# Performance work log

Measured on AMD Instinct MI355X. Metric: run time of the kernel, lower is better.

## Reference

```python
import jax, jax.numpy as jnp
import numpy as np

B, N, S = 8, 8192, 128


def setup_inputs() -> dict:
    key = jax.random.key(0)
    k1, k2, k3 = jax.random.split(key, 3)
    densities = jax.random.uniform(k1, (B, N, S, 1), dtype=jnp.float32)
    rgbs = jax.random.uniform(k2, (B, N, S, 3), dtype=jnp.float32)
    # sample distances along each ray must be increasing -> sort along S
    t_vals = jnp.sort(jax.random.uniform(k3, (B, N, S), dtype=jnp.float32) * 6.0, axis=-1)
    return {"densities": densities, "rgbs": rgbs, "t_vals": t_vals}


def reference(densities, rgbs, t_vals):
    INF_DELTA = 1e10
    EPS = 1e-10
    sigma = densities[..., 0]                                   # [B,N,S]
    deltas = t_vals[..., 1:] - t_vals[..., :-1]
    deltas = jnp.concatenate(
        [deltas, jnp.full_like(deltas[..., :1], INF_DELTA)], axis=-1
    )                                                           # [B,N,S]
    alpha = 1.0 - jnp.exp(-sigma * deltas)                      # [B,N,S]
    # exclusive cumprod of (1 - alpha): T_i = prod_{j<i} (1 - alpha_j)
    trans = jnp.cumprod(
        jnp.concatenate([jnp.ones_like(alpha[..., :1]), 1.0 - alpha + EPS], axis=-1),
        axis=-1,
    )[..., :-1]                                                 # [B,N,S]
    weights = trans * alpha                                     # [B,N,S]
    rgb = jnp.einsum("bns,bnsc->bnc", weights, rgbs)            # [B,N,3]
    depth = jnp.sum(weights * t_vals, axis=-1, keepdims=True)   # [B,N,1]
    accumulation = jnp.sum(weights, axis=-1, keepdims=True)     # [B,N,1]
    return rgb, weights, depth, accumulation
```

## Files before the change

kernel.cpp:

```cpp
#include <hip/hip_runtime.h>


namespace {
constexpr int kB = 8;
constexpr int kN = 8192;
constexpr int kS = 128;
constexpr int kRays = kB * kN;
constexpr int kWavesPerBlock = 4;

__global__ __launch_bounds__(256) void volrender_kernel(
    const float* __restrict__ dens,
    const float* __restrict__ rgbs,
    const float* __restrict__ tvals,
    float* __restrict__ out_rgb,
    float* __restrict__ out_w,
    float* __restrict__ out_depth,
    float* __restrict__ out_acc)
{
    const int lane = threadIdx.x & 63;
    const int wave = threadIdx.x >> 6;
    const int ray  = blockIdx.x * kWavesPerBlock + wave;

    const long base = (long)ray * kS;

    const float2 t2 = *(const float2*)(tvals + base + lane * 2);
    const float2 sg = *(const float2*)(dens  + base + lane * 2);
    const float* rp = rgbs + (long)ray * kS * 3 + lane * 6;
    const float2 ra = *(const float2*)(rp + 0);
    const float2 rb = *(const float2*)(rp + 2);
    const float2 rc = *(const float2*)(rp + 4);

    const float t_next = __shfl_down(t2.x, 1);
    const float d0 = t2.y - t2.x;
    const float d1 = (lane == 63) ? 1e10f : (t_next - t2.y);

    const float e0 = expf(-sg.x * d0);
    const float e1 = expf(-sg.y * d1);
    const float a0 = 1.0f - e0;
    const float a1 = 1.0f - e1;
    const float f0 = e0 + 1e-10f;
    const float f1 = e1 + 1e-10f;

    float p = f0 * f1;
    #pragma unroll
    for (int off = 1; off < 64; off <<= 1) {
        const float q = __shfl_up(p, off);
        if (lane >= off) p *= q;
    }
    float excl = __shfl_up(p, 1);
    if (lane == 0) excl = 1.0f;

    const float T0 = excl;
    const float T1 = excl * f0;
    const float w0 = T0 * a0;
    const float w1 = T1 * a1;

    *(float2*)(out_w + base + lane * 2) = make_float2(w0, w1);

    float cr  = w0 * ra.x + w1 * rb.y;
    float cg  = w0 * ra.y + w1 * rc.x;
    float cb  = w0 * rb.x + w1 * rc.y;
    float dep = w0 * t2.x + w1 * t2.y;
    float acc = w0 + w1;

    #pragma unroll
    for (int off = 32; off; off >>= 1) {
        cr  += __shfl_down(cr,  off);
        cg  += __shfl_down(cg,  off);
        cb  += __shfl_down(cb,  off);
        dep += __shfl_down(dep, off);
        acc += __shfl_down(acc, off);
    }

    if (lane == 0) {
        out_rgb[ray * 3 + 0] = cr;
        out_rgb[ray * 3 + 1] = cg;
        out_rgb[ray * 3 + 2] = cb;
        out_depth[ray] = dep;
        out_acc[ray]   = acc;
    }
}
}

extern "C" void kernel_launch(void* const* d_in, const int* in_sizes, int n_in,
                              void* d_out, int out_size, void* d_ws, size_t ws_size,
                              hipStream_t stream) {
    const float* dens  = (const float*)d_in[0];
    const float* rgbs  = (const float*)d_in[1];
    const float* tvals = (const float*)d_in[2];

    float* out       = (float*)d_out;
    float* out_rgb   = out;
    float* out_w     = out_rgb + (long)kRays * 3;
    float* out_depth = out_w + (long)kRays * kS;
    float* out_acc   = out_depth + kRays;

    const dim3 grid(kRays / kWavesPerBlock);
    const dim3 block(kWavesPerBlock * 64);
    hipLaunchKernelGGL(volrender_kernel, grid, block, 0, stream,
                       dens, rgbs, tvals, out_rgb, out_w, out_depth, out_acc);
}
```

Before: 34.84 us.

## Process two rays per wave with four samples per lane using float4 loads

Each 64-lane wave now handles two rays: 32 lanes per ray, 4 samples per lane. Loads and the weights store widen to float4, and the prefix-product scan and reductions shrink to 5 steps with xor shuffles. expf is replaced by the faster __expf. This halves the grid and cuts shuffle and scan overhead per sample, at the cost of more registers per lane and slightly lower exp precision.

```diff
diff --git a/kernel.cpp b/kernel.cpp
--- a/kernel.cpp
+++ b/kernel.cpp
@@ -19,60 +19,67 @@
 {
     const int lane = threadIdx.x & 63;
     const int wave = threadIdx.x >> 6;
-    const int ray  = blockIdx.x * kWavesPerBlock + wave;
+    const int seg  = lane & 31;
+    const int ray  = (blockIdx.x * kWavesPerBlock + wave) * 2 + (lane >> 5);
 
-    const long base = (long)ray * kS;
+    const long base = (long)ray * kS + seg * 4;
 
-    const float2 t2 = *(const float2*)(tvals + base + lane * 2);
-    const float2 sg = *(const float2*)(dens  + base + lane * 2);
-    const float* rp = rgbs + (long)ray * kS * 3 + lane * 6;
-    const float2 ra = *(const float2*)(rp + 0);
-    const float2 rb = *(const float2*)(rp + 2);
-    const float2 rc = *(const float2*)(rp + 4);
+    const float4 t4 = *(const float4*)(tvals + base);
+    const float4 s4 = *(const float4*)(dens  + base);
+    const float* rp = rgbs + (long)ray * kS * 3 + seg * 12;
+    const float4 q0 = *(const float4*)(rp + 0);
+    const float4 q1 = *(const float4*)(rp + 4);
+    const float4 q2 = *(const float4*)(rp + 8);
 
-    const float t_next = __shfl_down(t2.x, 1);
-    const float d0 = t2.y - t2.x;
-    const float d1 = (lane == 63) ? 1e10f : (t_next - t2.y);
+    const float t_next = __shfl_down(t4.x, 1);
+    const float d0 = t4.y - t4.x;
+    const float d1 = t4.z - t4.y;
+    const float d2 = t4.w - t4.z;
+    const float d3 = (seg == 31) ? 1e10f : (t_next - t4.w);
 
-    const float e0 = expf(-sg.x * d0);
-    const float e1 = expf(-sg.y * d1);
-    const float a0 = 1.0f - e0;
-    const float a1 = 1.0f - e1;
-    const float f0 = e0 + 1e-10f;
-    const float f1 = e1 + 1e-10f;
+    const float e0 = __expf(-s4.x * d0);
+    const float e1 = __expf(-s4.y * d1);
+    const float e2 = __expf(-s4.z * d2);
+    const float e3 = __expf(-s4.w * d3);
+    const float f0 = e0 + 1e-10f, f1 = e1 + 1e-10f;
+    const float f2 = e2 + 1e-10f, f3 = e3 + 1e-10f;
 
-    float p = f0 * f1;
+    float p = (f0 * f1) * (f2 * f3);
     #pragma unroll
-    for (int off = 1; off < 64; off <<= 1) {
+    for (int off = 1; off < 32; off <<= 1) {
         const float q = __shfl_up(p, off);
-        if (lane >= off) p *= q;
+        if (seg >= off) p *= q;
     }
     float excl = __shfl_up(p, 1);
-    if (lane == 0) excl = 1.0f;
+    if (seg == 0) excl = 1.0f;
 
     const float T0 = excl;
-    const float T1 = excl * f0;
-    const float w0 = T0 * a0;
-    const float w1 = T1 * a1;
+    const float T1 = T0 * f0;
+    const float T2 = T1 * f1;
+    const float T3 = T2 * f2;
+    const float w0 = T0 * (1.0f - e0);
+    const float w1 = T1 * (1.0f - e1);
+    const float w2 = T2 * (1.0f - e2);
+    const float w3 = T3 * (1.0f - e3);
 
-    *(float2*)(out_w + base + lane * 2) = make_float2(w0, w1);
+    *(float4*)(out_w + base) = make_float4(w0, w1, w2, w3);
 
-    float cr  = w0 * ra.x + w1 * rb.y;
-    float cg  = w0 * ra.y + w1 * rc.x;
-    float cb  = w0 * rb.x + w1 * rc.y;
-    float dep = w0 * t2.x + w1 * t2.y;
-    float acc = w0 + w1;
+    float cr  = w0 * q0.x + w1 * q0.w + w2 * q1.z + w3 * q2.y;
+    float cg  = w0 * q0.y + w1 * q1.x + w2 * q1.w + w3 * q2.z;
+    float cb  = w0 * q0.z + w1 * q1.y + w2 * q2.x + w3 * q2.w;
+    float dep = w0 * t4.x + w1 * t4.y + w2 * t4.z + w3 * t4.w;
+    float acc = w0 + w1 + w2 + w3;
 
     #pragma unroll
-    for (int off = 32; off; off >>= 1) {
-        cr  += __shfl_down(cr,  off);
-        cg  += __shfl_down(cg,  off);
-        cb  += __shfl_down(cb,  off);
-        dep += __shfl_down(dep, off);
-        acc += __shfl_down(acc, off);
+    for (int off = 16; off; off >>= 1) {
+        cr  += __shfl_xor(cr,  off);
+        cg  += __shfl_xor(cg,  off);
+        cb  += __shfl_xor(cb,  off);
+        dep += __shfl_xor(dep, off);
+        acc += __shfl_xor(acc, off);
     }
 
-    if (lane == 0) {
+    if (seg == 0) {
         out_rgb[ray * 3 + 0] = cr;
         out_rgb[ray * 3 + 1] = cg;
         out_rgb[ray * 3 + 2] = cb;
@@ -95,7 +102,7 @@
     float* out_depth = out_w + (long)kRays * kS;
     float* out_acc   = out_depth + kRays;
 
-    const dim3 grid(kRays / kWavesPerBlock);
+    const dim3 grid(kRays / (kWavesPerBlock * 2));
     const dim3 block(kWavesPerBlock * 64);
     hipLaunchKernelGGL(volrender_kernel, grid, block, 0, stream,
                        dens, rgbs, tvals, out_rgb, out_w, out_depth, out_acc);
```

Result: faster. 33.69 us (-3.3%).
